# Kernel tuning notes

Measured on AMD Instinct MI355X. Metric: run time of the kernel, lower is better.

The kernel has to match this reference:

```python
import jax, jax.numpy as jnp
import numpy as np


def setup_inputs() -> dict:
    key = jax.random.key(0)
    x = jax.random.normal(key, (256, 512, 1024), dtype=jnp.float32)
    return {"x": x}


def reference(x) -> jnp.ndarray:
    # Per-row (first dim) fake-quantization to int8 range, dequant, then ReLU.
    # Original torch code loops over rows; here we vectorize with keepdims reductions.
    red_axes = tuple(range(1, x.ndim))
    M = jnp.max(x, axis=red_axes, keepdims=True)  # per-row max (detached in original)
    m = jnp.min(x, axis=red_axes, keepdims=True)  # per-row min (detached in original)
    rng = M - m
    # quantize: round(254*(x-m)/(M-m) - 127) / 1000   (the /1000, *1000 pair is kept for bit-faithfulness)
    q = jnp.round(254.0 * (x - m) / rng - 127.0) / 1000.0
    # dequantize: (1000*q + 127) * (M-m)/254 + m
    deq = (1000.0 * q + 127.0) * rng / 254.0 + m
    return jax.nn.relu(deq)
```

## Files before the change

### kernel.cpp

```cpp
#include <hip/hip_runtime.h>
#include <math.h>

constexpr int ROWS    = 256;
constexpr int ROWLEN  = 512 * 1024;
constexpr int CHUNKS  = 32;
constexpr int BLOCK   = 256;
constexpr int ROWF4   = ROWLEN / 4;
constexpr int CHUNKF4 = ROWF4 / CHUNKS;
constexpr int F4_PER_THREAD = CHUNKF4 / BLOCK;

__global__ __launch_bounds__(BLOCK) void rowminmax_partial(
    const float4* __restrict__ x,
    float* __restrict__ pmin, float* __restrict__ pmax) {
  const int bid   = blockIdx.x;
  const int row   = bid >> 5;
  const int chunk = bid & (CHUNKS - 1);
  const float4* p = x + (size_t)row * ROWF4 + (size_t)chunk * CHUNKF4;

  float vmin = INFINITY, vmax = -INFINITY;
#pragma unroll
  for (int i = 0; i < F4_PER_THREAD; ++i) {
    float4 v = p[threadIdx.x + i * BLOCK];
    vmin = fminf(vmin, fminf(fminf(v.x, v.y), fminf(v.z, v.w)));
    vmax = fmaxf(vmax, fmaxf(fmaxf(v.x, v.y), fmaxf(v.z, v.w)));
  }

#pragma unroll
  for (int off = 32; off > 0; off >>= 1) {
    vmin = fminf(vmin, __shfl_xor(vmin, off, 64));
    vmax = fmaxf(vmax, __shfl_xor(vmax, off, 64));
  }

  __shared__ float smin[BLOCK / 64], smax[BLOCK / 64];
  const int wave = threadIdx.x >> 6;
  const int lane = threadIdx.x & 63;
  if (lane == 0) { smin[wave] = vmin; smax[wave] = vmax; }
  __syncthreads();
  if (threadIdx.x == 0) {
    float a = smin[0], b = smax[0];
#pragma unroll
    for (int w = 1; w < BLOCK / 64; ++w) {
      a = fminf(a, smin[w]);
      b = fmaxf(b, smax[w]);
    }
    pmin[bid] = a;
    pmax[bid] = b;
  }
}

__global__ __launch_bounds__(BLOCK) void quant_relu(
    const float4* __restrict__ x, float4* __restrict__ out,
    const float* __restrict__ pmin, const float* __restrict__ pmax) {
  const int bid   = (int)gridDim.x - 1 - (int)blockIdx.x;
  const int row   = bid >> 5;
  const int chunk = bid & (CHUNKS - 1);

  float m = INFINITY, M = -INFINITY;
#pragma unroll
  for (int i = 0; i < CHUNKS; ++i) {
    m = fminf(m, pmin[row * CHUNKS + i]);
    M = fmaxf(M, pmax[row * CHUNKS + i]);
  }
  const float rng   = M - m;
  const float scale = 254.0f / rng;
  const float step  = rng / 254.0f;

  const float4* p = x   + (size_t)row * ROWF4 + (size_t)chunk * CHUNKF4;
  float4*       q = out + (size_t)row * ROWF4 + (size_t)chunk * CHUNKF4;

#pragma unroll 4
  for (int i = 0; i < F4_PER_THREAD; ++i) {
    float4 v = p[threadIdx.x + i * BLOCK];
    float4 o;
    o.x = fmaxf(fmaf(rintf(fmaf(v.x - m, scale, -127.0f)) + 127.0f, step, m), 0.0f);
    o.y = fmaxf(fmaf(rintf(fmaf(v.y - m, scale, -127.0f)) + 127.0f, step, m), 0.0f);
    o.z = fmaxf(fmaf(rintf(fmaf(v.z - m, scale, -127.0f)) + 127.0f, step, m), 0.0f);
    o.w = fmaxf(fmaf(rintf(fmaf(v.w - m, scale, -127.0f)) + 127.0f, step, m), 0.0f);
    q[threadIdx.x + i * BLOCK] = o;
  }
}

extern "C" void kernel_launch(void* const* d_in, const int* in_sizes, int n_in,
                              void* d_out, int out_size, void* d_ws, size_t ws_size,
                              hipStream_t stream) {
  const float4* x   = (const float4*)d_in[0];
  float4*       out = (float4*)d_out;
  float*        pmin = (float*)d_ws;
  float*        pmax = pmin + ROWS * CHUNKS;

  rowminmax_partial<<<ROWS * CHUNKS, BLOCK, 0, stream>>>((const float4*)x, pmin, pmax);
  quant_relu<<<ROWS * CHUNKS, BLOCK, 0, stream>>>(x, out, pmin, pmax);
}
```

Baseline: 945.7 us.

## Fuse min/max and quantize passes into one cooperative kernel with grid sync

Result: slower. 1.365 ms (+44.3%).

```diff
diff --git a/kernel.cpp b/kernel.cpp
--- a/kernel.cpp
+++ b/kernel.cpp
@@ -1,93 +1,87 @@
 #include <hip/hip_runtime.h>
+#include <hip/hip_cooperative_groups.h>
 #include <math.h>
+
+namespace cg = cooperative_groups;
+
+typedef float nfloat4 __attribute__((ext_vector_type(4)));
 
 constexpr int ROWS    = 256;
 constexpr int ROWLEN  = 512 * 1024;
-constexpr int CHUNKS  = 32;
 constexpr int BLOCK   = 256;
+constexpr int GRID    = 1024;
+constexpr int BPR     = GRID / ROWS;
 constexpr int ROWF4   = ROWLEN / 4;
-constexpr int CHUNKF4 = ROWF4 / CHUNKS;
-constexpr int F4_PER_THREAD = CHUNKF4 / BLOCK;
+constexpr int CHUNKF4 = ROWF4 / BPR;
+constexpr int FPT     = CHUNKF4 / BLOCK;
 
-__global__ __launch_bounds__(BLOCK) void rowminmax_partial(
-    const float4* __restrict__ x,
+__global__ __launch_bounds__(BLOCK, 4) void fused_quant_relu(
+    const float4* __restrict__ x, float4* __restrict__ out,
     float* __restrict__ pmin, float* __restrict__ pmax) {
-  const int bid   = blockIdx.x;
-  const int row   = bid >> 5;
-  const int chunk = bid & (CHUNKS - 1);
-  const float4* p = x + (size_t)row * ROWF4 + (size_t)chunk * CHUNKF4;
+  const int bid = blockIdx.x;
+  const int row = bid / BPR;
+  const int sub = bid % BPR;
+  const int tid = threadIdx.x;
+  const float4* p = x + (size_t)row * ROWF4 + (size_t)sub * CHUNKF4;
 
   float vmin = INFINITY, vmax = -INFINITY;
-#pragma unroll
-  for (int i = 0; i < F4_PER_THREAD; ++i) {
-    float4 v = p[threadIdx.x + i * BLOCK];
+#pragma unroll 8
+  for (int i = 0; i < FPT; ++i) {
+    float4 v = p[tid + i * BLOCK];
     vmin = fminf(vmin, fminf(fminf(v.x, v.y), fminf(v.z, v.w)));
     vmax = fmaxf(vmax, fmaxf(fmaxf(v.x, v.y), fmaxf(v.z, v.w)));
   }
-
 #pragma unroll
   for (int off = 32; off > 0; off >>= 1) {
     vmin = fminf(vmin, __shfl_xor(vmin, off, 64));
     vmax = fmaxf(vmax, __shfl_xor(vmax, off, 64));
   }
-
   __shared__ float smin[BLOCK / 64], smax[BLOCK / 64];
-  const int wave = threadIdx.x >> 6;
-  const int lane = threadIdx.x & 63;
+  const int wave = tid >> 6, lane = tid & 63;
   if (lane == 0) { smin[wave] = vmin; smax[wave] = vmax; }
   __syncthreads();
-  if (threadIdx.x == 0) {
-    float a = smin[0], b = smax[0];
-#pragma unroll
-    for (int w = 1; w < BLOCK / 64; ++w) {
-      a = fminf(a, smin[w]);
-      b = fmaxf(b, smax[w]);
-    }
-    pmin[bid] = a;
-    pmax[bid] = b;
+  if (tid == 0) {
+    float a = fminf(fminf(smin[0], smin[1]), fminf(smin[2], smin[3]));
+    float b = fmaxf(fmaxf(smax[0], smax[1]), fmaxf(smax[2], smax[3]));
+    __hip_atomic_store(&pmin[bid], a, __ATOMIC_RELEASE, __HIP_MEMORY_SCOPE_AGENT);
+    __hip_atomic_store(&pmax[bid], b, __ATOMIC_RELEASE, __HIP_MEMORY_SCOPE_AGENT);
   }
-}
 
-__global__ __launch_bounds__(BLOCK) void quant_relu(
-    const float4* __restrict__ x, float4* __restrict__ out,
-    const float* __restrict__ pmin, const float* __restrict__ pmax) {
-  const int bid   = (int)gridDim.x - 1 - (int)blockIdx.x;
-  const int row   = bid >> 5;
-  const int chunk = bid & (CHUNKS - 1);
+  cg::this_grid().sync();
 
   float m = INFINITY, M = -INFINITY;
 #pragma unroll
-  for (int i = 0; i < CHUNKS; ++i) {
-    m = fminf(m, pmin[row * CHUNKS + i]);
-    M = fmaxf(M, pmax[row * CHUNKS + i]);
+  for (int i = 0; i < BPR; ++i) {
+    m = fminf(m, __hip_atomic_load(&pmin[row * BPR + i], __ATOMIC_ACQUIRE, __HIP_MEMORY_SCOPE_AGENT));
+    M = fmaxf(M, __hip_atomic_load(&pmax[row * BPR + i], __ATOMIC_ACQUIRE, __HIP_MEMORY_SCOPE_AGENT));
   }
   const float rng   = M - m;
   const float scale = 254.0f / rng;
   const float step  = rng / 254.0f;
 
-  const float4* p = x   + (size_t)row * ROWF4 + (size_t)chunk * CHUNKF4;
-  float4*       q = out + (size_t)row * ROWF4 + (size_t)chunk * CHUNKF4;
-
+  nfloat4* q = (nfloat4*)(out + (size_t)row * ROWF4 + (size_t)sub * CHUNKF4);
 #pragma unroll 4
-  for (int i = 0; i < F4_PER_THREAD; ++i) {
-    float4 v = p[threadIdx.x + i * BLOCK];
-    float4 o;
+  for (int i = FPT - 1; i >= 0; --i) {
+    const int idx = tid + i * BLOCK;
+    float4 v = p[idx];
+    nfloat4 o;
     o.x = fmaxf(fmaf(rintf(fmaf(v.x - m, scale, -127.0f)) + 127.0f, step, m), 0.0f);
     o.y = fmaxf(fmaf(rintf(fmaf(v.y - m, scale, -127.0f)) + 127.0f, step, m), 0.0f);
     o.z = fmaxf(fmaf(rintf(fmaf(v.z - m, scale, -127.0f)) + 127.0f, step, m), 0.0f);
     o.w = fmaxf(fmaf(rintf(fmaf(v.w - m, scale, -127.0f)) + 127.0f, step, m), 0.0f);
-    q[threadIdx.x + i * BLOCK] = o;
+    __builtin_nontemporal_store(o, &q[idx]);
   }
 }
 
 extern "C" void kernel_launch(void* const* d_in, const int* in_sizes, int n_in,
                               void* d_out, int out_size, void* d_ws, size_t ws_size,
                               hipStream_t stream) {
-  const float4* x   = (const float4*)d_in[0];
-  float4*       out = (float4*)d_out;
+  const float4* x    = (const float4*)d_in[0];
+  float4*       out  = (float4*)d_out;
   float*        pmin = (float*)d_ws;
-  float*        pmax = pmin + ROWS * CHUNKS;
+  float*        pmax = pmin + GRID;
 
-  rowminmax_partial<<<ROWS * CHUNKS, BLOCK, 0, stream>>>((const float4*)x, pmin, pmax);
-  quant_relu<<<ROWS * CHUNKS, BLOCK, 0, stream>>>(x, out, pmin, pmax);
+  void* args[] = {(void*)&x, (void*)&out, (void*)&pmin, (void*)&pmax};
+  (void)hipLaunchCooperativeKernel((void*)fused_quant_relu, dim3(GRID), dim3(BLOCK),
+                                   args, 0, stream);
 }
```
